# Kernel optimization log

Measured on AMD Instinct MI355X. Metric: run time of the kernel, lower is better.

The kernel has to match this reference:

```python
import jax, jax.numpy as jnp
import numpy as np

N = 2560          # 64 graphs * 40 nodes (hard-coded by view(64,40,40))
E = 163840        # edges, avg degree 64
HEADS = 4
IN_C = 32
H0 = 128          # hidden_dims[0] per head
H1 = 128          # hidden_dims[1] per head
OUT_E = 40
EPS_BN = 1e-5


def _glorot(key, shape):
    fan = sum(shape[-2:]) if len(shape) > 1 else shape[0]
    return jax.random.normal(key, shape, dtype=jnp.float32) * (2.0 / fan) ** 0.5


def setup_inputs() -> dict:
    key = jax.random.key(0)
    ks = jax.random.split(key, 24)
    inp = {
        "x": jax.random.normal(ks[0], (N, IN_C), dtype=jnp.float32),
        "edge_index": jax.random.randint(ks[1], (2, E), 0, N, dtype=jnp.int32),
        "pos": jax.random.normal(ks[2], (N, 2), dtype=jnp.float32),
        "mask": jax.random.randint(ks[3], (N,), 0, 2, dtype=jnp.int32),
        "adjacency": jax.random.uniform(ks[4], (N, OUT_E), dtype=jnp.float32),
        # GAT layer 1 (in -> heads*H0)
        "W1": _glorot(ks[5], (IN_C, HEADS * H0)),
        "att_src1": _glorot(ks[6], (HEADS, H0)),
        "att_dst1": _glorot(ks[7], (HEADS, H0)),
        "We1": _glorot(ks[8], (1, HEADS * H0)),
        "att_e1": _glorot(ks[9], (HEADS, H0)),
        "bias1": jnp.zeros((HEADS * H0,), dtype=jnp.float32),
        # BatchNorm 1
        "g1": jnp.ones((HEADS * H0,), dtype=jnp.float32),
        "be1": jnp.zeros((HEADS * H0,), dtype=jnp.float32),
        # GAT layer 2 (heads*H0 -> heads*H1)
        "W2": _glorot(ks[10], (HEADS * H0, HEADS * H1)),
        "att_src2": _glorot(ks[11], (HEADS, H1)),
        "att_dst2": _glorot(ks[12], (HEADS, H1)),
        "We2": _glorot(ks[13], (1, HEADS * H1)),
        "att_e2": _glorot(ks[14], (HEADS, H1)),
        "bias2": jnp.zeros((HEADS * H1,), dtype=jnp.float32),
        # BatchNorm 2
        "g2": jnp.ones((HEADS * H1,), dtype=jnp.float32),
        "be2": jnp.zeros((HEADS * H1,), dtype=jnp.float32),
        # fc_edge
        "Wfc": _glorot(ks[15], (HEADS * H1, OUT_E)),
        "bfc": jnp.zeros((OUT_E,), dtype=jnp.float32),
    }
    return inp


def _gat(x, src, dst, ew, W, att_s, att_d, We, att_e, bias, heads, c):
    # x: [N, Fin] -> h: [N, H, C]
    h = (x @ W).reshape(-1, heads, c)
    a_s = (h * att_s).sum(-1)                       # [N, H]
    a_d = (h * att_d).sum(-1)                       # [N, H]
    he = (ew[:, None] @ We).reshape(-1, heads, c)   # [E, H, C] edge attr proj
    a_e = (he * att_e).sum(-1)                      # [E, H]
    alpha = jax.nn.leaky_relu(a_s[src] + a_d[dst] + a_e, 0.2)
    # segment softmax over destination nodes
    m = jax.ops.segment_max(alpha, dst, num_segments=N)
    alpha = jnp.exp(alpha - m[dst])
    denom = jax.ops.segment_sum(alpha, dst, num_segments=N)
    alpha = alpha / (denom[dst] + 1e-16)
    out = jax.ops.segment_sum(h[src] * alpha[:, :, None], dst, num_segments=N)
    return out.reshape(-1, heads * c) + bias


def _batchnorm(x, g, b):
    mu = x.mean(0)
    var = x.var(0)
    return (x - mu) * jax.lax.rsqrt(var + EPS_BN) * g + b


def reference(x, edge_index, pos, mask, adjacency,
              W1, att_src1, att_dst1, We1, att_e1, bias1, g1, be1,
              W2, att_src2, att_dst2, We2, att_e2, bias2, g2, be2,
              Wfc, bfc):
    src, dst = edge_index[0], edge_index[1]
    ew = 1.0 / (jnp.linalg.norm(pos[src] - pos[dst], axis=1) + 1e-6)  # [E]

    h = _gat(x, src, dst, ew, W1, att_src1, att_dst1, We1, att_e1, bias1, HEADS, H0)
    h = jax.nn.relu(_batchnorm(h, g1, be1))

    e = _gat(h, src, dst, ew, W2, att_src2, att_dst2, We2, att_e2, bias2, HEADS, H1)
    e = jax.nn.relu(_batchnorm(e, g2, be2))

    out_edge = e @ Wfc + bfc                     # [N, 40]
    out_edge = out_edge * mask[:, None].astype(out_edge.dtype)
    out_edge = out_edge.reshape(64, 40, 40)
    return out_edge + adjacency.reshape(64, 40, 40)
```

## Files before the change

kernel.cpp:

```cpp
#include <hip/hip_runtime.h>
#include <hip/hip_bf16.h>

#define NN 2560
#define NE 163840
#define NH 4
#define NC 128
#define NF 512
#define OUTE 40
#define CSTR 256

typedef short bf16x8 __attribute__((ext_vector_type(8)));
typedef float f32x4 __attribute__((ext_vector_type(4)));

__device__ inline ushort f2bf(float f) {
    uint u = __float_as_uint(f);
    uint r = u + 0x7FFF + ((u >> 16) & 1);
    return (ushort)(r >> 16);
}
__device__ inline float bflo(uint v) { return __uint_as_float(v << 16); }
__device__ inline float bfhi(uint v) { return __uint_as_float(v & 0xFFFF0000u); }
__device__ inline float bf2f(ushort u) { return __uint_as_float(((uint)u) << 16); }
__device__ inline float rdlanef(float v, int l) {
    return __int_as_float(__builtin_amdgcn_readlane(__float_as_int(v), l));
}
__device__ inline int rdlanei(int v, int l) {
    return __builtin_amdgcn_readlane(v, l);
}

__global__ __launch_bounds__(256) void k_csr_gemm1(const int* __restrict__ ei,
        const float* __restrict__ pos, int* __restrict__ deg,
        int2* __restrict__ csrp, int* __restrict__ ovf_cnt, int4* __restrict__ ovf,
        const float* __restrict__ We1, const float* __restrict__ ae1,
        const float* __restrict__ We2, const float* __restrict__ ae2,
        float* __restrict__ dote,
        const float* __restrict__ Wfc, ushort* __restrict__ WfcT,
        const float* __restrict__ W2, ushort* __restrict__ W2T,
        const float* __restrict__ x, const float* __restrict__ W1,
        const float* __restrict__ atts, const float* __restrict__ attd,
        ushort* __restrict__ hb, float* __restrict__ as_, float* __restrict__ ad_) {
    __shared__ ushort tile[64][72];
    __shared__ float s_x[4][32];
    __shared__ float4 s_red[4][4];
    int b = blockIdx.x;
    if (b < 640) {
        int e = b * 256 + threadIdx.x;
        int s = ei[e], d = ei[NE + e];
        float dx = pos[2 * s] - pos[2 * d];
        float dy = pos[2 * s + 1] - pos[2 * d + 1];
        float w = 1.0f / (sqrtf(dx * dx + dy * dy) + 1e-6f);
        int r = atomicAdd(&deg[d], 1);
        if (r < CSTR) {
            csrp[(d << 8) + r] = make_int2(s, __float_as_int(w));
        } else {
            int i = atomicAdd(ovf_cnt, 1);
            ovf[i] = make_int4(d, s, __float_as_int(w), 0);
        }
        return;
    }
    if (b < 642) {
        int t = threadIdx.x;
        const float* W = (b == 641) ? We2 : We1;
        const float* A = (b == 641) ? ae2 : ae1;
        int w = t >> 6, l = t & 63;
        float p = W[w * 128 + l] * A[w * 128 + l] + W[w * 128 + 64 + l] * A[w * 128 + 64 + l];
#pragma unroll
        for (int o = 32; o > 0; o >>= 1) p += __shfl_down(p, o);
        if (l == 0) dote[(b - 640) * 4 + w] = p;
        return;
    }
    if (b < 738) {
        int idx = (b - 642) * 256 + threadIdx.x;
        int j = idx >> 9, k = idx & 511;
        WfcT[idx] = (j < OUTE) ? f2bf(Wfc[k * OUTE + j]) : (ushort)0;
        return;
    }
    if (b < 802) {
        int id = b - 738;
        int n0 = (id & 7) * 64, k0 = (id >> 3) * 64;
        int t = threadIdx.x;
        int r = t >> 2, cseg = (t & 3) * 16;
#pragma unroll
        for (int c = 0; c < 16; c += 4) {
            float4 v = *(const float4*)&W2[(k0 + r) * 512 + n0 + cseg + c];
            tile[cseg + c + 0][r] = f2bf(v.x);
            tile[cseg + c + 1][r] = f2bf(v.y);
            tile[cseg + c + 2][r] = f2bf(v.z);
            tile[cseg + c + 3][r] = f2bf(v.w);
        }
        __syncthreads();
        *(uint4*)&W2T[(n0 + r) * 512 + k0 + cseg]     = *(uint4*)&tile[r][cseg];
        *(uint4*)&W2T[(n0 + r) * 512 + k0 + cseg + 8] = *(uint4*)&tile[r][cseg + 8];
        return;
    }
    int n0 = (b - 802) * 4, t = threadIdx.x;
    if (t < 128) s_x[t >> 5][t & 31] = x[n0 * 32 + t];
    __syncthreads();
    float a0[4] = {0.f, 0.f, 0.f, 0.f}, a1[4] = {0.f, 0.f, 0.f, 0.f};
#pragma unroll
    for (int k = 0; k < 32; k++) {
        float w0 = W1[k * 512 + t];
        float w1 = W1[k * 512 + t + 256];
#pragma unroll
        for (int nn = 0; nn < 4; nn++) {
            a0[nn] += s_x[nn][k] * w0;
            a1[nn] += s_x[nn][k] * w1;
        }
    }
    float sa0 = atts[t], sa1 = atts[t + 256];
    float da0 = attd[t], da1 = attd[t + 256];
    int w = t >> 6, lane = t & 63;
#pragma unroll
    for (int nn = 0; nn < 4; nn++) {
        hb[(n0 + nn) * 512 + t] = f2bf(a0[nn]);
        hb[(n0 + nn) * 512 + t + 256] = f2bf(a1[nn]);
        float ps0 = a0[nn] * sa0, pd0 = a0[nn] * da0;
        float ps1 = a1[nn] * sa1, pd1 = a1[nn] * da1;
#pragma unroll
        for (int o = 32; o > 0; o >>= 1) {
            ps0 += __shfl_xor(ps0, o); pd0 += __shfl_xor(pd0, o);
            ps1 += __shfl_xor(ps1, o); pd1 += __shfl_xor(pd1, o);
        }
        if (lane == 0) s_red[w][nn] = make_float4(ps0, pd0, ps1, pd1);
    }
    __syncthreads();
    if (t < 4) {
        int nn = t, n = n0 + nn;
        float4 r0 = s_red[0][nn], r1 = s_red[1][nn], r2 = s_red[2][nn], r3 = s_red[3][nn];
        as_[n * 4 + 0] = r0.x + r1.x; as_[n * 4 + 1] = r2.x + r3.x;
        as_[n * 4 + 2] = r0.z + r1.z; as_[n * 4 + 3] = r2.z + r3.z;
        ad_[n * 4 + 0] = r0.y + r1.y; ad_[n * 4 + 1] = r2.y + r3.y;
        ad_[n * 4 + 2] = r0.w + r1.w; ad_[n * 4 + 3] = r2.w + r3.w;
    }
}

__global__ __launch_bounds__(256) void k_edge_agg(const int* __restrict__ deg_,
        const int2* __restrict__ csrp, const int* __restrict__ ovf_cnt,
        const int4* __restrict__ ovf, const float* __restrict__ as_,
        const float* __restrict__ ad_, const float* __restrict__ dote,
        const ushort* __restrict__ hb, const float* __restrict__ bias,
        ushort* __restrict__ outb) {
    int w = threadIdx.x >> 6, lane = threadIdx.x & 63;
    int n = blockIdx.x * 2 + (w >> 1);
    int hp = w & 1;
    int h0 = 2 * hp;
    int beg = n << 8;
    int degn = deg_[n];
    int dmain = min(degn, CSTR);
    float ad0 = ad_[n * 4 + h0], ad1 = ad_[n * 4 + h0 + 1];
    float d0 = dote[h0], d1 = dote[h0 + 1];
    float La0 = -1e30f, La1 = -1e30f, Lb0 = -1e30f, Lb1 = -1e30f;
    int off0 = 0, off1 = 0;
    if (lane < dmain) {
        int2 p = csrp[beg + lane];
        off0 = p.x * NF;
        float2 a = *(const float2*)&as_[p.x * 4 + h0];
        float ww = __int_as_float(p.y);
        float v0 = a.x + ad0 + ww * d0; La0 = v0 > 0.f ? v0 : 0.2f * v0;
        float v1 = a.y + ad1 + ww * d1; La1 = v1 > 0.f ? v1 : 0.2f * v1;
    }
    if (lane + 64 < dmain) {
        int2 p = csrp[beg + lane + 64];
        off1 = p.x * NF;
        float2 a = *(const float2*)&as_[p.x * 4 + h0];
        float ww = __int_as_float(p.y);
        float v0 = a.x + ad0 + ww * d0; Lb0 = v0 > 0.f ? v0 : 0.2f * v0;
        float v1 = a.y + ad1 + ww * d1; Lb1 = v1 > 0.f ? v1 : 0.2f * v1;
    }
    float mx0 = fmaxf(La0, Lb0), mx1 = fmaxf(La1, Lb1);
    for (int e = 128 + lane; e < dmain; e += 64) {
        int2 p = csrp[beg + e];
        float2 a = *(const float2*)&as_[p.x * 4 + h0];
        float ww = __int_as_float(p.y);
        float v0 = a.x + ad0 + ww * d0; v0 = v0 > 0.f ? v0 : 0.2f * v0;
        float v1 = a.y + ad1 + ww * d1; v1 = v1 > 0.f ? v1 : 0.2f * v1;
        mx0 = fmaxf(mx0, v0); mx1 = fmaxf(mx1, v1);
    }
    if (degn > CSTR) {
        int oc = *ovf_cnt;
        for (int i = lane; i < oc; i += 64) {
            int4 o = ovf[i];
            if (o.x == n) {
                float2 a = *(const float2*)&as_[o.y * 4 + h0];
                float ww = __int_as_float(o.z);
                float v0 = a.x + ad0 + ww * d0; v0 = v0 > 0.f ? v0 : 0.2f * v0;
                float v1 = a.y + ad1 + ww * d1; v1 = v1 > 0.f ? v1 : 0.2f * v1;
                mx0 = fmaxf(mx0, v0); mx1 = fmaxf(mx1, v1);
            }
        }
    }
#pragma unroll
    for (int o = 32; o > 0; o >>= 1) {
        mx0 = fmaxf(mx0, __shfl_xor(mx0, o));
        mx1 = fmaxf(mx1, __shfl_xor(mx1, o));
    }
    float Aa0 = __expf(La0 - mx0), Ab0 = __expf(Lb0 - mx0);
    float Aa1 = __expf(La1 - mx1), Ab1 = __expf(Lb1 - mx1);
    float s0 = Aa0 + Ab0, s1 = Aa1 + Ab1;
    for (int e = 128 + lane; e < dmain; e += 64) {
        int2 p = csrp[beg + e];
        float2 a = *(const float2*)&as_[p.x * 4 + h0];
        float ww = __int_as_float(p.y);
        float v0 = a.x + ad0 + ww * d0; v0 = v0 > 0.f ? v0 : 0.2f * v0;
        float v1 = a.y + ad1 + ww * d1; v1 = v1 > 0.f ? v1 : 0.2f * v1;
        s0 += __expf(v0 - mx0); s1 += __expf(v1 - mx1);
    }
    if (degn > CSTR) {
        int oc = *ovf_cnt;
        for (int i = lane; i < oc; i += 64) {
            int4 o = ovf[i];
            if (o.x == n) {
                float2 a = *(const float2*)&as_[o.y * 4 + h0];
                float ww = __int_as_float(o.z);
                float v0 = a.x + ad0 + ww * d0; v0 = v0 > 0.f ? v0 : 0.2f * v0;
                float v1 = a.y + ad1 + ww * d1; v1 = v1 > 0.f ? v1 : 0.2f * v1;
                s0 += __expf(v0 - mx0); s1 += __expf(v1 - mx1);
            }
        }
    }
#pragma unroll
    for (int o = 32; o > 0; o >>= 1) {
        s0 += __shfl_xor(s0, o); s1 += __shfl_xor(s1, o);
    }
    float inv0 = 1.f / (s0 + 1e-16f), inv1 = 1.f / (s1 + 1e-16f);
    bool hi = lane >= 32;
    const ushort* hbase = hb + hp * 256 + 4 * lane;
    float4 acc = make_float4(0.f, 0.f, 0.f, 0.f);
    int m0 = min(dmain, 64);
#pragma unroll 16
    for (int e = 0; e < m0; e++) {
        float al = rdlanef(Aa0, e), ah = rdlanef(Aa1, e);
        float a = hi ? ah : al;
        int o = rdlanei(off0, e);
        uint2 v = *(const uint2*)(hbase + o);
        acc.x += a * bflo(v.x); acc.y += a * bfhi(v.x);
        acc.z += a * bflo(v.y); acc.w += a * bfhi(v.y);
    }
    int m1 = min(dmain, 128);
#pragma unroll 16
    for (int e = 64; e < m1; e++) {
        float al = rdlanef(Ab0, e - 64), ah = rdlanef(Ab1, e - 64);
        float a = hi ? ah : al;
        int o = rdlanei(off1, e - 64);
        uint2 v = *(const uint2*)(hbase + o);
        acc.x += a * bflo(v.x); acc.y += a * bfhi(v.x);
        acc.z += a * bflo(v.y); acc.w += a * bfhi(v.y);
    }
    for (int e = 128; e < dmain; e++) {
        int2 p = csrp[beg + e];
        float2 aa = *(const float2*)&as_[p.x * 4 + h0];
        float ww = __int_as_float(p.y);
        float v0 = aa.x + ad0 + ww * d0; v0 = v0 > 0.f ? v0 : 0.2f * v0;
        float v1 = aa.y + ad1 + ww * d1; v1 = v1 > 0.f ? v1 : 0.2f * v1;
        float a = hi ? __expf(v1 - mx1) : __expf(v0 - mx0);
        uint2 v = *(const uint2*)(hbase + p.x * NF);
        acc.x += a * bflo(v.x); acc.y += a * bfhi(v.x);
        acc.z += a * bflo(v.y); acc.w += a * bfhi(v.y);
    }
    if (degn > CSTR) {
        int oc = *ovf_cnt;
        for (int i = 0; i < oc; i++) {
            int4 o = ovf[i];
            if (o.x == n) {
                float2 aa = *(const float2*)&as_[o.y * 4 + h0];
                float ww = __int_as_float(o.z);
                float v0 = aa.x + ad0 + ww * d0; v0 = v0 > 0.f ? v0 : 0.2f * v0;
                float v1 = aa.y + ad1 + ww * d1; v1 = v1 > 0.f ? v1 : 0.2f * v1;
                float a = hi ? __expf(v1 - mx1) : __expf(v0 - mx0);
                uint2 v = *(const uint2*)(hbase + o.y * NF);
                acc.x += a * bflo(v.x); acc.y += a * bfhi(v.x);
                acc.z += a * bflo(v.y); acc.w += a * bfhi(v.y);
            }
        }
    }
    float inv = hi ? inv1 : inv0;
    int ch = hp * 256 + 4 * lane;
    float4 b4 = *(const float4*)&bias[ch];
    ushort4 o4;
    o4.x = f2bf(acc.x * inv + b4.x); o4.y = f2bf(acc.y * inv + b4.y);
    o4.z = f2bf(acc.z * inv + b4.z); o4.w = f2bf(acc.w * inv + b4.w);
    *(ushort4*)&outb[n * NF + ch] = o4;
}

__global__ void k_bnstats(const ushort* __restrict__ x, float* __restrict__ stats) {
    int t = threadIdx.x;
    int r0 = blockIdx.x * 16;
    float s = 0.f, s2 = 0.f;
    for (int r = r0; r < r0 + 16; r++) {
        float v = bf2f(x[r * NF + t]);
        s += v; s2 += v * v;
    }
    atomicAdd(&stats[t], s);
    atomicAdd(&stats[NF + t], s2);
}

__global__ __launch_bounds__(256) void k_gemm2_bn_att(const ushort* __restrict__ Ab,
        const float* __restrict__ stats, const float* __restrict__ g,
        const float* __restrict__ bb, const ushort* __restrict__ BT,
        const float* __restrict__ atts, const float* __restrict__ attd,
        ushort* __restrict__ Cb, float* __restrict__ as_, float* __restrict__ ad_) {
    __shared__ ushort As[64][40];
    __shared__ ushort Bs[128][40];
    __shared__ float s_scale[512], s_shift[512];
    __shared__ float s_ps[2][64], s_pd[2][64];
    int t = threadIdx.x;
    const float invn = 1.0f / (float)NN;
    {
        int j = t;
#pragma unroll
        for (int rep = 0; rep < 2; rep++, j += 256) {
            float mu = stats[j] * invn;
            float var = stats[NF + j] * invn - mu * mu;
            float sc = rsqrtf(var + 1e-5f) * g[j];
            s_scale[j] = sc;
            s_shift[j] = bb[j] - mu * sc;
        }
    }
    int head = blockIdx.x;
    int rowBase = blockIdx.y * 64, colBase = head * 128;
    int w = t >> 6, lane = t & 63;
    int wm = (w >> 1) * 32, wn = (w & 1) * 64;
    int lm = lane & 15, q = lane >> 4;
    f32x4 acc[2][4] = {};
    int sr2 = t >> 2, sk = (t & 3) * 8;
    for (int k0 = 0; k0 < 512; k0 += 32) {
        __syncthreads();
        int jb = k0 + sk;
        float sc[8], sh[8];
#pragma unroll
        for (int c = 0; c < 8; c++) { sc[c] = s_scale[jb + c]; sh[c] = s_shift[jb + c]; }
        uint4 a8 = *(const uint4*)&Ab[(rowBase + sr2) * 512 + jb];
        uint4 b0 = *(const uint4*)&BT[(colBase + sr2) * 512 + jb];
        uint4 b1 = *(const uint4*)&BT[(colBase + 64 + sr2) * 512 + jb];
        ushort pa0[8];
        float av[8];
        av[0] = bflo(a8.x); av[1] = bfhi(a8.x); av[2] = bflo(a8.y); av[3] = bfhi(a8.y);
        av[4] = bflo(a8.z); av[5] = bfhi(a8.z); av[6] = bflo(a8.w); av[7] = bfhi(a8.w);
#pragma unroll
        for (int c = 0; c < 8; c++)
            pa0[c] = f2bf(fmaxf(av[c] * sc[c] + sh[c], 0.f));
        *(uint4*)&As[sr2][sk]      = *(uint4*)pa0;
        *(uint4*)&Bs[sr2][sk]      = b0;
        *(uint4*)&Bs[64 + sr2][sk] = b1;
        __syncthreads();
        bf16x8 af[2], bf[4];
#pragma unroll
        for (int i = 0; i < 2; i++) af[i] = *(const bf16x8*)&As[wm + i * 16 + lm][q * 8];
#pragma unroll
        for (int j = 0; j < 4; j++) bf[j] = *(const bf16x8*)&Bs[wn + j * 16 + lm][q * 8];
#pragma unroll
        for (int i = 0; i < 2; i++)
#pragma unroll
            for (int j = 0; j < 4; j++)
                acc[i][j] = __builtin_amdgcn_mfma_f32_16x16x32_bf16(af[i], bf[j], acc[i][j], 0, 0, 0);
    }
#pragma unroll
    for (int i = 0; i < 2; i++) {
        int row = rowBase + wm + i * 16 + q * 4;
#pragma unroll
        for (int j = 0; j < 4; j++) {
            int col = colBase + wn + j * 16 + lm;
#pragma unroll
            for (int r = 0; r < 4; r++)
                Cb[(row + r) * 512 + col] = f2bf(acc[i][j][r]);
        }
    }
    float sa[4], da[4];
#pragma unroll
    for (int j = 0; j < 4; j++) {
        int col = colBase + wn + j * 16 + lm;
        sa[j] = atts[col]; da[j] = attd[col];
    }
#pragma unroll
    for (int i = 0; i < 2; i++) {
#pragma unroll
        for (int r = 0; r < 4; r++) {
            float ps = 0.f, pd = 0.f;
#pragma unroll
            for (int j = 0; j < 4; j++) {
                float c = acc[i][j][r];
                ps += c * sa[j]; pd += c * da[j];
            }
#pragma unroll
            for (int o = 1; o < 16; o <<= 1) { ps += __shfl_xor(ps, o); pd += __shfl_xor(pd, o); }
            if (lm == 0) {
                int row = wm + i * 16 + q * 4 + r;
                s_ps[w & 1][row] = ps; s_pd[w & 1][row] = pd;
            }
        }
    }
    __syncthreads();
    if (t < 64) {
        as_[(rowBase + t) * 4 + head] = s_ps[0][t] + s_ps[1][t];
    } else if (t < 128) {
        int row = t - 64;
        ad_[(rowBase + row) * 4 + head] = s_pd[0][row] + s_pd[1][row];
    }
}

__global__ __launch_bounds__(256) void k_fc_bn(const ushort* __restrict__ e2b,
        const float* __restrict__ stats, const float* __restrict__ g,
        const float* __restrict__ bb, const ushort* __restrict__ WfcT,
        const float* __restrict__ bfc, const int* __restrict__ mask,
        const float* __restrict__ adj, float* __restrict__ out) {
    __shared__ float s_scale[512], s_shift[512];
    __shared__ f32x4 s_acc[3][64][3];
    int t = threadIdx.x;
    int w = t >> 6, lane = t & 63;
    const float invn = 1.0f / (float)NN;
#pragma unroll
    for (int j = t; j < 512; j += 256) {
        float mu = stats[j] * invn;
        float var = stats[NF + j] * invn - mu * mu;
        float sc = rsqrtf(var + 1e-5f) * g[j];
        s_scale[j] = sc;
        s_shift[j] = bb[j] - mu * sc;
    }
    __syncthreads();
    int r0 = blockIdx.x * 16;
    int lm = lane & 15, q = lane >> 4;
    f32x4 acc[3] = {};
#pragma unroll
    for (int kk = 0; kk < 4; kk++) {
        int k0 = w * 128 + kk * 32;
        int jb = k0 + q * 8;
        uint4 a8 = *(const uint4*)&e2b[(r0 + lm) * 512 + jb];
        float av[8];
        av[0] = bflo(a8.x); av[1] = bfhi(a8.x); av[2] = bflo(a8.y); av[3] = bfhi(a8.y);
        av[4] = bflo(a8.z); av[5] = bfhi(a8.z); av[6] = bflo(a8.w); av[7] = bfhi(a8.w);
        ushort pa[8];
#pragma unroll
        for (int c = 0; c < 8; c++)
            pa[c] = f2bf(fmaxf(av[c] * s_scale[jb + c] + s_shift[jb + c], 0.f));
        bf16x8 af = *(const bf16x8*)pa;
#pragma unroll
        for (int jt = 0; jt < 3; jt++) {
            bf16x8 bf = *(const bf16x8*)&WfcT[(jt * 16 + lm) * 512 + k0 + q * 8];
            acc[jt] = __builtin_amdgcn_mfma_f32_16x16x32_bf16(af, bf, acc[jt], 0, 0, 0);
        }
    }
    if (w > 0) {
#pragma unroll
        for (int jt = 0; jt < 3; jt++) s_acc[w - 1][lane][jt] = acc[jt];
    }
    __syncthreads();
    if (w == 0) {
#pragma unroll
        for (int jt = 0; jt < 3; jt++) {
            acc[jt] += s_acc[0][lane][jt] + s_acc[1][lane][jt] + s_acc[2][lane][jt];
            int col = jt * 16 + lm;
            if (col < OUTE) {
#pragma unroll
                for (int r = 0; r < 4; r++) {
                    int n = r0 + q * 4 + r;
                    float v = acc[jt][r] + bfc[col];
                    v = mask[n] ? v : 0.f;
                    out[n * OUTE + col] = v + adj[n * OUTE + col];
                }
            }
        }
    }
}

extern "C" void kernel_launch(void* const* d_in, const int* in_sizes, int n_in,
                              void* d_out, int out_size, void* d_ws, size_t ws_size,
                              hipStream_t stream) {
    const float* x       = (const float*)d_in[0];
    const int*   ei      = (const int*)d_in[1];
    const float* pos     = (const float*)d_in[2];
    const int*   mask    = (const int*)d_in[3];
    const float* adj     = (const float*)d_in[4];
    const float* W1      = (const float*)d_in[5];
    const float* atts1   = (const float*)d_in[6];
    const float* attd1   = (const float*)d_in[7];
    const float* We1     = (const float*)d_in[8];
    const float* atte1   = (const float*)d_in[9];
    const float* bias1   = (const float*)d_in[10];
    const float* g1      = (const float*)d_in[11];
    const float* be1     = (const float*)d_in[12];
    const float* W2      = (const float*)d_in[13];
    const float* atts2   = (const float*)d_in[14];
    const float* attd2   = (const float*)d_in[15];
    const float* We2     = (const float*)d_in[16];
    const float* atte2   = (const float*)d_in[17];
    const float* bias2   = (const float*)d_in[18];
    const float* g2      = (const float*)d_in[19];
    const float* be2     = (const float*)d_in[20];
    const float* Wfc     = (const float*)d_in[21];
    const float* bfc     = (const float*)d_in[22];
    float* out = (float*)d_out;

    char* ws = (char*)d_ws;
    int*    deg     = (int*)(ws);
    int*    ovf_cnt = (int*)(ws + 2560 * 4);
    float*  stats   = (float*)(ws + 5120 * 4);
    float*  dote    = (float*)(ws + 7168 * 4);
    int2*   csrp    = (int2*)(ws + 7184 * 4);
    int4*   ovf     = (int4*)(ws + 1317904 * 4);
    float*  as_     = (float*)(ws + 1973264 * 4);
    float*  ad_     = (float*)(ws + 1983504 * 4);
    ushort* t1b     = (ushort*)(ws + 1993744 * 4);
    ushort* hb      = (ushort*)(ws + 2649104 * 4);
    ushort* W2T     = (ushort*)(ws + 3304464 * 4);
    ushort* WfcT    = (ushort*)(ws + 3435536 * 4);

    hipMemsetAsync(d_ws, 0, 7168 * 4, stream);

    k_csr_gemm1<<<802 + NN / 4, 256, 0, stream>>>(ei, pos, deg, csrp, ovf_cnt, ovf,
                                                  We1, atte1, We2, atte2, dote,
                                                  Wfc, WfcT, W2, W2T,
                                                  x, W1, atts1, attd1, hb, as_, ad_);

    k_edge_agg<<<NN / 2, 256, 0, stream>>>(deg, csrp, ovf_cnt, ovf, as_, ad_,
                                           dote, hb, bias1, t1b);
    k_bnstats<<<NN / 16, 512, 0, stream>>>(t1b, stats);

    k_gemm2_bn_att<<<dim3(4, NN / 64), 256, 0, stream>>>(t1b, stats, g1, be1, W2T,
                                                         atts2, attd2, hb, as_, ad_);
    k_edge_agg<<<NN / 2, 256, 0, stream>>>(deg, csrp, ovf_cnt, ovf, as_, ad_,
                                           dote + 4, hb, bias2, t1b);
    k_bnstats<<<NN / 16, 512, 0, stream>>>(t1b, stats + 1024);

    k_fc_bn<<<NN / 16, 256, 0, stream>>>(t1b, stats + 1024, g2, be2, WfcT, bfc, mask, adj, out);
}
```

Baseline: 204.3 us.

## Process all four heads per wave in edge aggregation and vectorize BN stats

The edge aggregation kernel now assigns one wave per node covering all four heads, with each lane holding 8 channels, instead of two waves per node handling two heads each. Softmax logits, max and sum are computed once per edge for all heads, so the per-edge index and as_ loads and the max/sum passes are no longer duplicated across two waves. Gathers widen to 16-byte loads and the block size drops to 128 threads. The BN stats kernel switches to 8-channel vector loads with a shared-memory reduction, which is meant to cut atomics and load instructions, at the cost of more registers per lane.

```diff
diff --git a/kernel.cpp b/kernel.cpp
--- a/kernel.cpp
+++ b/kernel.cpp
@@ -25,6 +25,9 @@
 }
 __device__ inline int rdlanei(int v, int l) {
     return __builtin_amdgcn_readlane(v, l);
+}
+__device__ inline float sel4(float r0, float r1, float r2, float r3, int hd) {
+    return (hd & 2) ? ((hd & 1) ? r3 : r2) : ((hd & 1) ? r1 : r0);
 }
 
 __global__ __launch_bounds__(256) void k_csr_gemm1(const int* __restrict__ ei,
@@ -133,58 +136,68 @@
     }
 }
 
-__global__ __launch_bounds__(256) void k_edge_agg(const int* __restrict__ deg_,
+__global__ __launch_bounds__(128) void k_edge_agg(const int* __restrict__ deg_,
         const int2* __restrict__ csrp, const int* __restrict__ ovf_cnt,
         const int4* __restrict__ ovf, const float* __restrict__ as_,
         const float* __restrict__ ad_, const float* __restrict__ dote,
         const ushort* __restrict__ hb, const float* __restrict__ bias,
         ushort* __restrict__ outb) {
     int w = threadIdx.x >> 6, lane = threadIdx.x & 63;
-    int n = blockIdx.x * 2 + (w >> 1);
-    int hp = w & 1;
-    int h0 = 2 * hp;
+    int n = blockIdx.x * 2 + w;
     int beg = n << 8;
     int degn = deg_[n];
     int dmain = min(degn, CSTR);
-    float ad0 = ad_[n * 4 + h0], ad1 = ad_[n * 4 + h0 + 1];
-    float d0 = dote[h0], d1 = dote[h0 + 1];
-    float La0 = -1e30f, La1 = -1e30f, Lb0 = -1e30f, Lb1 = -1e30f;
+    float4 adv = *(const float4*)&ad_[n * 4];
+    float4 dv  = *(const float4*)dote;
+    float La0 = -1e30f, La1 = -1e30f, La2 = -1e30f, La3 = -1e30f;
+    float Lb0 = -1e30f, Lb1 = -1e30f, Lb2 = -1e30f, Lb3 = -1e30f;
     int off0 = 0, off1 = 0;
     if (lane < dmain) {
         int2 p = csrp[beg + lane];
         off0 = p.x * NF;
-        float2 a = *(const float2*)&as_[p.x * 4 + h0];
+        float4 a = *(const float4*)&as_[p.x * 4];
         float ww = __int_as_float(p.y);
-        float v0 = a.x + ad0 + ww * d0; La0 = v0 > 0.f ? v0 : 0.2f * v0;
-        float v1 = a.y + ad1 + ww * d1; La1 = v1 > 0.f ? v1 : 0.2f * v1;
+        float v0 = a.x + adv.x + ww * dv.x; La0 = v0 > 0.f ? v0 : 0.2f * v0;
+        float v1 = a.y + adv.y + ww * dv.y; La1 = v1 > 0.f ? v1 : 0.2f * v1;
+        float v2 = a.z + adv.z + ww * dv.z; La2 = v2 > 0.f ? v2 : 0.2f * v2;
+        float v3 = a.w + adv.w + ww * dv.w; La3 = v3 > 0.f ? v3 : 0.2f * v3;
     }
     if (lane + 64 < dmain) {
         int2 p = csrp[beg + lane + 64];
         off1 = p.x * NF;
-        float2 a = *(const float2*)&as_[p.x * 4 + h0];
+        float4 a = *(const float4*)&as_[p.x * 4];
         float ww = __int_as_float(p.y);
-        float v0 = a.x + ad0 + ww * d0; Lb0 = v0 > 0.f ? v0 : 0.2f * v0;
-        float v1 = a.y + ad1 + ww * d1; Lb1 = v1 > 0.f ? v1 : 0.2f * v1;
+        float v0 = a.x + adv.x + ww * dv.x; Lb0 = v0 > 0.f ? v0 : 0.2f * v0;
+        float v1 = a.y + adv.y + ww * dv.y; Lb1 = v1 > 0.f ? v1 : 0.2f * v1;
+        float v2 = a.z + adv.z + ww * dv.z; Lb2 = v2 > 0.f ? v2 : 0.2f * v2;
+        float v3 = a.w + adv.w + ww * dv.w; Lb3 = v3 > 0.f ? v3 : 0.2f * v3;
     }
     float mx0 = fmaxf(La0, Lb0), mx1 = fmaxf(La1, Lb1);
+    float mx2 = fmaxf(La2, Lb2), mx3 = fmaxf(La3, Lb3);
     for (int e = 128 + lane; e < dmain; e += 64) {
         int2 p = csrp[beg + e];
-        float2 a = *(const float2*)&as_[p.x * 4 + h0];
+        float4 a = *(const float4*)&as_[p.x * 4];
         float ww = __int_as_float(p.y);
-        float v0 = a.x + ad0 + ww * d0; v0 = v0 > 0.f ? v0 : 0.2f * v0;
-        float v1 = a.y + ad1 + ww * d1; v1 = v1 > 0.f ? v1 : 0.2f * v1;
+        float v0 = a.x + adv.x + ww * dv.x; v0 = v0 > 0.f ? v0 : 0.2f * v0;
+        float v1 = a.y + adv.y + ww * dv.y; v1 = v1 > 0.f ? v1 : 0.2f * v1;
+        float v2 = a.z + adv.z + ww * dv.z; v2 = v2 > 0.f ? v2 : 0.2f * v2;
+        float v3 = a.w + adv.w + ww * dv.w; v3 = v3 > 0.f ? v3 : 0.2f * v3;
         mx0 = fmaxf(mx0, v0); mx1 = fmaxf(mx1, v1);
+        mx2 = fmaxf(mx2, v2); mx3 = fmaxf(mx3, v3);
     }
     if (degn > CSTR) {
         int oc = *ovf_cnt;
         for (int i = lane; i < oc; i += 64) {
             int4 o = ovf[i];
             if (o.x == n) {
-                float2 a = *(const float2*)&as_[o.y * 4 + h0];
+                float4 a = *(const float4*)&as_[o.y * 4];
                 float ww = __int_as_float(o.z);
-                float v0 = a.x + ad0 + ww * d0; v0 = v0 > 0.f ? v0 : 0.2f * v0;
-                float v1 = a.y + ad1 + ww * d1; v1 = v1 > 0.f ? v1 : 0.2f * v1;
+                float v0 = a.x + adv.x + ww * dv.x; v0 = v0 > 0.f ? v0 : 0.2f * v0;
+                float v1 = a.y + adv.y + ww * dv.y; v1 = v1 > 0.f ? v1 : 0.2f * v1;
+                float v2 = a.z + adv.z + ww * dv.z; v2 = v2 > 0.f ? v2 : 0.2f * v2;
+                float v3 = a.w + adv.w + ww * dv.w; v3 = v3 > 0.f ? v3 : 0.2f * v3;
                 mx0 = fmaxf(mx0, v0); mx1 = fmaxf(mx1, v1);
+                mx2 = fmaxf(mx2, v2); mx3 = fmaxf(mx3, v3);
             }
         }
     }
@@ -192,105 +205,151 @@
     for (int o = 32; o > 0; o >>= 1) {
         mx0 = fmaxf(mx0, __shfl_xor(mx0, o));
         mx1 = fmaxf(mx1, __shfl_xor(mx1, o));
-    }
-    float Aa0 = __expf(La0 - mx0), Ab0 = __expf(Lb0 - mx0);
-    float Aa1 = __expf(La1 - mx1), Ab1 = __expf(Lb1 - mx1);
-    float s0 = Aa0 + Ab0, s1 = Aa1 + Ab1;
+        mx2 = fmaxf(mx2, __shfl_xor(mx2, o));
+        mx3 = fmaxf(mx3, __shfl_xor(mx3, o));
+    }
+    float Aa0 = __expf(La0 - mx0), Aa1 = __expf(La1 - mx1);
+    float Aa2 = __expf(La2 - mx2), Aa3 = __expf(La3 - mx3);
+    float Ab0 = __expf(Lb0 - mx0), Ab1 = __expf(Lb1 - mx1);
+    float Ab2 = __expf(Lb2 - mx2), Ab3 = __expf(Lb3 - mx3);
+    float s0 = Aa0 + Ab0, s1 = Aa1 + Ab1, s2 = Aa2 + Ab2, s3 = Aa3 + Ab3;
     for (int e = 128 + lane; e < dmain; e += 64) {
         int2 p = csrp[beg + e];
-        float2 a = *(const float2*)&as_[p.x * 4 + h0];
+        float4 a = *(const float4*)&as_[p.x * 4];
         float ww = __int_as_float(p.y);
-        float v0 = a.x + ad0 + ww * d0; v0 = v0 > 0.f ? v0 : 0.2f * v0;
-        float v1 = a.y + ad1 + ww * d1; v1 = v1 > 0.f ? v1 : 0.2f * v1;
+        float v0 = a.x + adv.x + ww * dv.x; v0 = v0 > 0.f ? v0 : 0.2f * v0;
+        float v1 = a.y + adv.y + ww * dv.y; v1 = v1 > 0.f ? v1 : 0.2f * v1;
+        float v2 = a.z + adv.z + ww * dv.z; v2 = v2 > 0.f ? v2 : 0.2f * v2;
+        float v3 = a.w + adv.w + ww * dv.w; v3 = v3 > 0.f ? v3 : 0.2f * v3;
         s0 += __expf(v0 - mx0); s1 += __expf(v1 - mx1);
+        s2 += __expf(v2 - mx2); s3 += __expf(v3 - mx3);
     }
     if (degn > CSTR) {
         int oc = *ovf_cnt;
         for (int i = lane; i < oc; i += 64) {
             int4 o = ovf[i];
             if (o.x == n) {
-                float2 a = *(const float2*)&as_[o.y * 4 + h0];
+                float4 a = *(const float4*)&as_[o.y * 4];
                 float ww = __int_as_float(o.z);
-                float v0 = a.x + ad0 + ww * d0; v0 = v0 > 0.f ? v0 : 0.2f * v0;
-                float v1 = a.y + ad1 + ww * d1; v1 = v1 > 0.f ? v1 : 0.2f * v1;
+                float v0 = a.x + adv.x + ww * dv.x; v0 = v0 > 0.f ? v0 : 0.2f * v0;
+                float v1 = a.y + adv.y + ww * dv.y; v1 = v1 > 0.f ? v1 : 0.2f * v1;
+                float v2 = a.z + adv.z + ww * dv.z; v2 = v2 > 0.f ? v2 : 0.2f * v2;
+                float v3 = a.w + adv.w + ww * dv.w; v3 = v3 > 0.f ? v3 : 0.2f * v3;
                 s0 += __expf(v0 - mx0); s1 += __expf(v1 - mx1);
+                s2 += __expf(v2 - mx2); s3 += __expf(v3 - mx3);
             }
         }
     }
 #pragma unroll
     for (int o = 32; o > 0; o >>= 1) {
         s0 += __shfl_xor(s0, o); s1 += __shfl_xor(s1, o);
+        s2 += __shfl_xor(s2, o); s3 += __shfl_xor(s3, o);
     }
     float inv0 = 1.f / (s0 + 1e-16f), inv1 = 1.f / (s1 + 1e-16f);
-    bool hi = lane >= 32;
-    const ushort* hbase = hb + hp * 256 + 4 * lane;
-    float4 acc = make_float4(0.f, 0.f, 0.f, 0.f);
+    float inv2 = 1.f / (s2 + 1e-16f), inv3 = 1.f / (s3 + 1e-16f);
+    int hd = lane >> 4;
+    const ushort* hbase = hb + 8 * lane;
+    float acc0 = 0.f, acc1 = 0.f, acc2 = 0.f, acc3 = 0.f;
+    float acc4 = 0.f, acc5 = 0.f, acc6 = 0.f, acc7 = 0.f;
     int m0 = min(dmain, 64);
 #pragma unroll 16
     for (int e = 0; e < m0; e++) {
-        float al = rdlanef(Aa0, e), ah = rdlanef(Aa1, e);
-        float a = hi ? ah : al;
+        float r0 = rdlanef(Aa0, e), r1 = rdlanef(Aa1, e);
+        float r2 = rdlanef(Aa2, e), r3 = rdlanef(Aa3, e);
+        float a = sel4(r0, r1, r2, r3, hd);
         int o = rdlanei(off0, e);
-        uint2 v = *(const uint2*)(hbase + o);
-        acc.x += a * bflo(v.x); acc.y += a * bfhi(v.x);
-        acc.z += a * bflo(v.y); acc.w += a * bfhi(v.y);
+        uint4 v = *(const uint4*)(hbase + o);
+        acc0 += a * bflo(v.x); acc1 += a * bfhi(v.x);
+        acc2 += a * bflo(v.y); acc3 += a * bfhi(v.y);
+        acc4 += a * bflo(v.z); acc5 += a * bfhi(v.z);
+        acc6 += a * bflo(v.w); acc7 += a * bfhi(v.w);
     }
     int m1 = min(dmain, 128);
 #pragma unroll 16
     for (int e = 64; e < m1; e++) {
-        float al = rdlanef(Ab0, e - 64), ah = rdlanef(Ab1, e - 64);
-        float a = hi ? ah : al;
+        float r0 = rdlanef(Ab0, e - 64), r1 = rdlanef(Ab1, e - 64);
+        float r2 = rdlanef(Ab2, e - 64), r3 = rdlanef(Ab3, e - 64);
+        float a = sel4(r0, r1, r2, r3, hd);
         int o = rdlanei(off1, e - 64);
-        uint2 v = *(const uint2*)(hbase + o);
-        acc.x += a * bflo(v.x); acc.y += a * bfhi(v.x);
-        acc.z += a * bflo(v.y); acc.w += a * bfhi(v.y);
-    }
+        uint4 v = *(const uint4*)(hbase + o);
+        acc0 += a * bflo(v.x); acc1 += a * bfhi(v.x);
+        acc2 += a * bflo(v.y); acc3 += a * bfhi(v.y);
+        acc4 += a * bflo(v.z); acc5 += a * bfhi(v.z);
+        acc6 += a * bflo(v.w); acc7 += a * bfhi(v.w);
+    }
+    float adh = sel4(adv.x, adv.y, adv.z, adv.w, hd);
+    float dh  = sel4(dv.x, dv.y, dv.z, dv.w, hd);
+    float mxh = sel4(mx0, mx1, mx2, mx3, hd);
+    float ash;
     for (int e = 128; e < dmain; e++) {
         int2 p = csrp[beg + e];
-        float2 aa = *(const float2*)&as_[p.x * 4 + h0];
+        ash = as_[p.x * 4 + hd];
         float ww = __int_as_float(p.y);
-        float v0 = aa.x + ad0 + ww * d0; v0 = v0 > 0.f ? v0 : 0.2f * v0;
-        float v1 = aa.y + ad1 + ww * d1; v1 = v1 > 0.f ? v1 : 0.2f * v1;
-        float a = hi ? __expf(v1 - mx1) : __expf(v0 - mx0);
-        uint2 v = *(const uint2*)(hbase + p.x * NF);
-        acc.x += a * bflo(v.x); acc.y += a * bfhi(v.x);
-        acc.z += a * bflo(v.y); acc.w += a * bfhi(v.y);
+        float vv = ash + adh + ww * dh; vv = vv > 0.f ? vv : 0.2f * vv;
+        float a = __expf(vv - mxh);
+        uint4 v = *(const uint4*)(hbase + p.x * NF);
+        acc0 += a * bflo(v.x); acc1 += a * bfhi(v.x);
+        acc2 += a * bflo(v.y); acc3 += a * bfhi(v.y);
+        acc4 += a * bflo(v.z); acc5 += a * bfhi(v.z);
+        acc6 += a * bflo(v.w); acc7 += a * bfhi(v.w);
     }
     if (degn > CSTR) {
         int oc = *ovf_cnt;
         for (int i = 0; i < oc; i++) {
             int4 o = ovf[i];
             if (o.x == n) {
-                float2 aa = *(const float2*)&as_[o.y * 4 + h0];
+                ash = as_[o.y * 4 + hd];
                 float ww = __int_as_float(o.z);
-                float v0 = aa.x + ad0 + ww * d0; v0 = v0 > 0.f ? v0 : 0.2f * v0;
-                float v1 = aa.y + ad1 + ww * d1; v1 = v1 > 0.f ? v1 : 0.2f * v1;
-                float a = hi ? __expf(v1 - mx1) : __expf(v0 - mx0);
-                uint2 v = *(const uint2*)(hbase + o.y * NF);
-                acc.x += a * bflo(v.x); acc.y += a * bfhi(v.x);
-                acc.z += a * bflo(v.y); acc.w += a * bfhi(v.y);
+                float vv = ash + adh + ww * dh; vv = vv > 0.f ? vv : 0.2f * vv;
+                float a = __expf(vv - mxh);
+                uint4 v = *(const uint4*)(hbase + o.y * NF);
+                acc0 += a * bflo(v.x); acc1 += a * bfhi(v.x);
+                acc2 += a * bflo(v.y); acc3 += a * bfhi(v.y);
+                acc4 += a * bflo(v.z); acc5 += a * bfhi(v.z);
+                acc6 += a * bflo(v.w); acc7 += a * bfhi(v.w);
             }
         }
     }
-    float inv = hi ? inv1 : inv0;
-    int ch = hp * 256 + 4 * lane;
-    float4 b4 = *(const float4*)&bias[ch];
-    ushort4 o4;
-    o4.x = f2bf(acc.x * inv + b4.x); o4.y = f2bf(acc.y * inv + b4.y);
-    o4.z = f2bf(acc.z * inv + b4.z); o4.w = f2bf(acc.w * inv + b4.w);
-    *(ushort4*)&outb[n * NF + ch] = o4;
-}
-
-__global__ void k_bnstats(const ushort* __restrict__ x, float* __restrict__ stats) {
+    float invh = sel4(inv0, inv1, inv2, inv3, hd);
+    int ch = 8 * lane;
+    float4 b0 = *(const float4*)&bias[ch];
+    float4 b1 = *(const float4*)&bias[ch + 4];
+    uint4 ov;
+    ov.x = (uint)f2bf(acc0 * invh + b0.x) | ((uint)f2bf(acc1 * invh + b0.y) << 16);
+    ov.y = (uint)f2bf(acc2 * invh + b0.z) | ((uint)f2bf(acc3 * invh + b0.w) << 16);
+    ov.z = (uint)f2bf(acc4 * invh + b1.x) | ((uint)f2bf(acc5 * invh + b1.y) << 16);
+    ov.w = (uint)f2bf(acc6 * invh + b1.z) | ((uint)f2bf(acc7 * invh + b1.w) << 16);
+    *(uint4*)&outb[n * NF + ch] = ov;
+}
+
+__global__ __launch_bounds__(256) void k_bnstats(const ushort* __restrict__ xs,
+        float* __restrict__ stats) {
+    __shared__ float ps[2048];
+    __shared__ float pq[2048];
     int t = threadIdx.x;
-    int r0 = blockIdx.x * 16;
-    float s = 0.f, s2 = 0.f;
-    for (int r = r0; r < r0 + 16; r++) {
-        float v = bf2f(x[r * NF + t]);
-        s += v; s2 += v * v;
-    }
-    atomicAdd(&stats[t], s);
-    atomicAdd(&stats[NF + t], s2);
+    int c8 = (t & 63) * 8, rr = t >> 6;
+    float s[8] = {0.f,0.f,0.f,0.f,0.f,0.f,0.f,0.f};
+    float q[8] = {0.f,0.f,0.f,0.f,0.f,0.f,0.f,0.f};
+#pragma unroll
+    for (int rj = 0; rj < 4; rj++) {
+        int r = blockIdx.x * 16 + rr * 4 + rj;
+        uint4 v = *(const uint4*)&xs[r * NF + c8];
+        float vv[8];
+        vv[0] = bflo(v.x); vv[1] = bfhi(v.x); vv[2] = bflo(v.y); vv[3] = bfhi(v.y);
+        vv[4] = bflo(v.z); vv[5] = bfhi(v.z); vv[6] = bflo(v.w); vv[7] = bfhi(v.w);
+#pragma unroll
+        for (int c = 0; c < 8; c++) { s[c] += vv[c]; q[c] += vv[c] * vv[c]; }
+    }
+#pragma unroll
+    for (int c = 0; c < 8; c++) {
+        ps[rr * 512 + c8 + c] = s[c];
+        pq[rr * 512 + c8 + c] = q[c];
+    }
+    __syncthreads();
+    for (int ch = t; ch < 512; ch += 256) {
+        atomicAdd(&stats[ch], ps[ch] + ps[512 + ch] + ps[1024 + ch] + ps[1536 + ch]);
+        atomicAdd(&stats[NF + ch], pq[ch] + pq[512 + ch] + pq[1024 + ch] + pq[1536 + ch]);
+    }
 }
 
 __global__ __launch_bounds__(256) void k_gemm2_bn_att(const ushort* __restrict__ Ab,
@@ -510,15 +569,15 @@
                                                   Wfc, WfcT, W2, W2T,
                                                   x, W1, atts1, attd1, hb, as_, ad_);
 
-    k_edge_agg<<<NN / 2, 256, 0, stream>>>(deg, csrp, ovf_cnt, ovf, as_, ad_,
+    k_edge_agg<<<NN / 2, 128, 0, stream>>>(deg, csrp, ovf_cnt, ovf, as_, ad_,
                                            dote, hb, bias1, t1b);
-    k_bnstats<<<NN / 16, 512, 0, stream>>>(t1b, stats);
+    k_bnstats<<<NN / 16, 256, 0, stream>>>(t1b, stats);
 
     k_gemm2_bn_att<<<dim3(4, NN / 64), 256, 0, stream>>>(t1b, stats, g1, be1, W2T,
                                                          atts2, attd2, hb, as_, ad_);
-    k_edge_agg<<<NN / 2, 256, 0, stream>>>(deg, csrp, ovf_cnt, ovf, as_, ad_,
+    k_edge_agg<<<NN / 2, 128, 0, stream>>>(deg, csrp, ovf_cnt, ovf, as_, ad_,
                                            dote + 4, hb, bias2, t1b);
-    k_bnstats<<<NN / 16, 512, 0, stream>>>(t1b, stats + 1024);
+    k_bnstats<<<NN / 16, 256, 0, stream>>>(t1b, stats + 1024);
 
     k_fc_bn<<<NN / 16, 256, 0, stream>>>(t1b, stats + 1024, g2, be2, WfcT, bfc, mask, adj, out);
 }
```

New measurement: 204.4 us. No clear change (+0.0%).
